# Optimization experiments

Measured on AMD Instinct MI355X. Metric: run time of the kernel, lower is better.

## Reference

```python
import jax, jax.numpy as jnp
import numpy as np

N_EMBD = 1024
N_HEAD = 16
HEAD_DIM = N_EMBD // N_HEAD


def _linear_params(key, fan_in, fan_out):
    kw, kb = jax.random.split(key)
    bound = 1.0 / np.sqrt(fan_in)
    W = jax.random.uniform(kw, (fan_out, fan_in), minval=-bound, maxval=bound, dtype=jnp.float32)
    b = jax.random.uniform(kb, (fan_out,), minval=-bound, maxval=bound, dtype=jnp.float32)
    return W, b


def setup_inputs() -> dict:
    key = jax.random.key(0)
    ks = jax.random.split(key, 7)
    B, T, C = 4, 2048, N_EMBD
    k = jax.random.normal(ks[0], (B, T, C), dtype=jnp.float32)
    q = jax.random.normal(ks[1], (B, T, C), dtype=jnp.float32)
    v = jax.random.normal(ks[2], (B, T, C), dtype=jnp.float32)
    Wk, bk = _linear_params(ks[3], C, C)
    Wq, bq = _linear_params(ks[4], C, C)
    Wv, bv = _linear_params(ks[5], C, C)
    Wo, bo = _linear_params(ks[6], C, C)
    return {"k": k, "q": q, "v": v, "Wk": Wk, "bk": bk, "Wq": Wq, "bq": bq,
            "Wv": Wv, "bv": bv, "Wo": Wo, "bo": bo}


def reference(k, q, v, Wk, bk, Wq, bq, Wv, bv, Wo, bo):
    B, T, C = k.shape
    H, CH = N_HEAD, C // N_HEAD
    # projections (nn.Linear: x @ W.T + b), split heads -> [b, h, t, ch]
    keys = (k @ Wk.T + bk).reshape(B, T, H, CH).transpose(0, 2, 1, 3)
    queries = (q @ Wq.T + bq).reshape(B, T, H, CH).transpose(0, 2, 1, 3)
    values = (v @ Wv.T + bv).reshape(B, T, H, CH).transpose(0, 2, 1, 3)
    # [b, h, t, t] scores, scaled before softmax as in the original
    att = jnp.einsum('bhqd,bhkd->bhqk', queries, keys)
    att = jax.nn.softmax(att * (CH ** -0.5), axis=-1)
    out = jnp.einsum('bhqk,bhkd->bhqd', att, values)
    out = out.transpose(0, 2, 1, 3).reshape(B, T, C)
    return out @ Wo.T + bo
```

## Files before the change

### kernel.cpp

```cpp
#include <hip/hip_runtime.h>


typedef short bf8 __attribute__((ext_vector_type(8)));
typedef float f4 __attribute__((ext_vector_type(4)));
typedef float f16v __attribute__((ext_vector_type(16)));
typedef unsigned short u16;

#define AS1 __attribute__((address_space(1)))
#define AS3 __attribute__((address_space(3)))

__device__ __forceinline__ u16 f2b(float f) {
  unsigned u = __builtin_bit_cast(unsigned, f);
  u += 0x7FFFu + ((u >> 16) & 1u);
  return (u16)(u >> 16);
}

__device__ __forceinline__ unsigned cvtpk(float lo, float hi) {
  unsigned r;
  asm("v_cvt_pk_bf16_f32 %0, %1, %2" : "=v"(r) : "v"(lo), "v"(hi));
  return r;
}

__device__ __forceinline__ void swap32(unsigned& a, unsigned& b) {
  asm("v_permlane32_swap_b32 %0, %1" : "+v"(a), "+v"(b));
}

__global__ void cvt4_kernel(const float* __restrict__ a, const float* __restrict__ b,
                            const float* __restrict__ c, const float* __restrict__ d,
                            u16* __restrict__ out) {
  int i = blockIdx.x * blockDim.x + threadIdx.x;
  const int sel = i >> 18, off = i & 0x3FFFF;
  const float* src = sel == 0 ? a : sel == 1 ? b : sel == 2 ? c : d;
  float4 f = ((const float4*)src)[off];
  ushort4 o;
  o.x = f2b(f.x); o.y = f2b(f.y); o.z = f2b(f.z); o.w = f2b(f.w);
  ((ushort4*)out)[i] = o;
}

template<int MODE>
__device__ __forceinline__ void gemm_epilogue(
    f4 (&acc)[4][4], const float* __restrict__ bias, void* __restrict__ Cout,
    int N, float scale, int m0, int n0, int wm, int wn, int lr, int lg)
{
  if (MODE == 0) {
    float bv[4];
    #pragma unroll
    for (int j = 0; j < 4; ++j) bv[j] = bias[n0 + wn + j * 16 + lr];
    float* C = (float*)Cout;
    #pragma unroll
    for (int i = 0; i < 4; ++i)
      #pragma unroll
      for (int j = 0; j < 4; ++j) {
        const int col = n0 + wn + j * 16 + lr;
        #pragma unroll
        for (int r = 0; r < 4; ++r) {
          const int row = m0 + wm + i * 16 + lg * 4 + r;
          C[(size_t)row * N + col] = acc[i][j][r] + bv[j];
        }
      }
  } else if (MODE == 1) {
    float bv[4];
    #pragma unroll
    for (int j = 0; j < 4; ++j) bv[j] = bias[n0 + wn + j * 16 + lr];
    u16* C = (u16*)Cout;
    #pragma unroll
    for (int i = 0; i < 4; ++i)
      #pragma unroll
      for (int j = 0; j < 4; ++j) {
        const int col = n0 + wn + j * 16 + lr;
        const int h = col >> 6, ch = col & 63;
        #pragma unroll
        for (int r = 0; r < 4; ++r) {
          const int row = m0 + wm + i * 16 + lg * 4 + r;
          const int b = row >> 11, t = row & 2047;
          C[((size_t)(b * 16 + h) * 2048 + t) * 64 + ch] = f2b((acc[i][j][r] + bv[j]) * scale);
        }
      }
  } else {
    u16* C = (u16*)Cout;
    #pragma unroll
    for (int i = 0; i < 4; ++i)
      #pragma unroll
      for (int r = 0; r < 4; ++r) {
        const int nch = m0 + wm + i * 16 + lg * 4 + r;
        const float br = bias[nch];
        const int h = nch >> 6, ch = nch & 63;
        #pragma unroll
        for (int j = 0; j < 4; ++j) {
          const int tok = n0 + wn + j * 16 + lr;
          const int b = tok >> 11, t = tok & 2047;
          C[((size_t)((b * 16 + h) * 64 + ch) << 11) + t] = f2b(acc[i][j][r] + br);
        }
      }
  }
}

template<int MODE, int ACTB>
__device__ __forceinline__ void gemm_fp_body(
    u16* __restrict__ actT, u16* __restrict__ wT,
    const float* __restrict__ act, const u16* __restrict__ Wt,
    const float* __restrict__ bias, void* __restrict__ Cout,
    int N, int K, float scale, int m0, int n0)
{
  const int tid = threadIdx.x, lane = tid & 63, w = tid >> 6;
  const int wm = (w >> 1) << 6, wn = (w & 1) << 6;
  const int lr = lane & 15, lg = lane >> 4;
  const int arow0 = (ACTB ? n0 : m0);
  const int wrow0 = (ACTB ? m0 : n0);

  f4 acc[4][4] = {};
  float4 ta[8];

  #pragma unroll
  for (int q = 0; q < 4; ++q) {
    const int c = (w << 8) + (q << 6) + lane;
    const int row = c >> 3, col = (c & 7) << 3;
    const float* s = act + (size_t)(arow0 + row) * K + col;
    ta[2 * q] = *(const float4*)s; ta[2 * q + 1] = *(const float4*)(s + 4);
  }
  #pragma unroll
  for (int q = 0; q < 4; ++q) {
    const int c = (w << 8) + (q << 6) + lane;
    const int row = c >> 3, sw = ((c & 7) ^ (row & 7)) << 3;
    __builtin_amdgcn_global_load_lds(
        (const AS1 void*)(Wt + (size_t)(wrow0 + row) * K + sw),
        (AS3 void*)(wT + (((w << 2) + q) << 9)), 16, 0, 0);
  }
  #pragma unroll
  for (int q = 0; q < 4; ++q) {
    const int c = (w << 8) + (q << 6) + lane;
    const int row = c >> 3;
    uint4 pk;
    pk.x = cvtpk(ta[2 * q].x, ta[2 * q].y);
    pk.y = cvtpk(ta[2 * q].z, ta[2 * q].w);
    pk.z = cvtpk(ta[2 * q + 1].x, ta[2 * q + 1].y);
    pk.w = cvtpk(ta[2 * q + 1].z, ta[2 * q + 1].w);
    *(uint4*)(actT + (row << 6) + (((c & 7) ^ (row & 7)) << 3)) = pk;
  }
  #pragma unroll
  for (int q = 0; q < 4; ++q) {
    const int c = (w << 8) + (q << 6) + lane;
    const int row = c >> 3, col = (c & 7) << 3;
    const float* s = act + (size_t)(arow0 + row) * K + 64 + col;
    ta[2 * q] = *(const float4*)s; ta[2 * q + 1] = *(const float4*)(s + 4);
  }
  __syncthreads();

  const int NKT = K >> 6;
  for (int kt = 0; kt < NKT; ++kt) {
    const int cur = kt & 1;
    const u16* aC = actT + (cur << 13);
    const u16* wC = wT + (cur << 13);
    if (kt + 1 < NKT) {
      u16* aN = actT + ((cur ^ 1) << 13);
      u16* wN = wT + ((cur ^ 1) << 13);
      const int k1 = (kt + 1) << 6;
      #pragma unroll
      for (int q = 0; q < 4; ++q) {
        const int c = (w << 8) + (q << 6) + lane;
        const int row = c >> 3, sw = ((c & 7) ^ (row & 7)) << 3;
        __builtin_amdgcn_global_load_lds(
            (const AS1 void*)(Wt + (size_t)(wrow0 + row) * K + k1 + sw),
            (AS3 void*)(wN + (((w << 2) + q) << 9)), 16, 0, 0);
      }
      #pragma unroll
      for (int q = 0; q < 4; ++q) {
        const int c = (w << 8) + (q << 6) + lane;
        const int row = c >> 3;
        uint4 pk;
        pk.x = cvtpk(ta[2 * q].x, ta[2 * q].y);
        pk.y = cvtpk(ta[2 * q].z, ta[2 * q].w);
        pk.z = cvtpk(ta[2 * q + 1].x, ta[2 * q + 1].y);
        pk.w = cvtpk(ta[2 * q + 1].z, ta[2 * q + 1].w);
        *(uint4*)(aN + (row << 6) + (((c & 7) ^ (row & 7)) << 3)) = pk;
      }
      if (kt + 2 < NKT) {
        const int k2 = (kt + 2) << 6;
        #pragma unroll
        for (int q = 0; q < 4; ++q) {
          const int c = (w << 8) + (q << 6) + lane;
          const int row = c >> 3, col = (c & 7) << 3;
          const float* s = act + (size_t)(arow0 + row) * K + k2 + col;
          ta[2 * q] = *(const float4*)s; ta[2 * q + 1] = *(const float4*)(s + 4);
        }
      }
    }
    #pragma unroll
    for (int ks = 0; ks < 2; ++ks) {
      bf8 af[4], bfr[4];
      #pragma unroll
      for (int i = 0; i < 4; ++i) {
        const int ra = wm + i * 16 + lr;
        const int rb = wn + i * 16 + lr;
        const u16* aSrc = ACTB ? wC : aC;
        const u16* bSrc = ACTB ? aC : wC;
        af[i]  = *(const bf8*)(aSrc + (ra << 6) + ((((ks << 2) + lg) ^ (ra & 7)) << 3));
        bfr[i] = *(const bf8*)(bSrc + (rb << 6) + ((((ks << 2) + lg) ^ (rb & 7)) << 3));
      }
      __builtin_amdgcn_s_setprio(1);
      #pragma unroll
      for (int i = 0; i < 4; ++i)
        #pragma unroll
        for (int j = 0; j < 4; ++j)
          acc[i][j] = __builtin_amdgcn_mfma_f32_16x16x32_bf16(af[i], bfr[j], acc[i][j], 0, 0, 0);
      __builtin_amdgcn_s_setprio(0);
    }
    __syncthreads();
  }

  gemm_epilogue<MODE>(acc, bias, Cout, N, scale, m0, n0, wm, wn, lr, lg);
}

__global__ __launch_bounds__(256, 2)
void proj_qkv(const float* __restrict__ q_in, const float* __restrict__ k_in,
              const float* __restrict__ v_in,
              const u16* __restrict__ Wq, const u16* __restrict__ Wk,
              const u16* __restrict__ Wv,
              const float* __restrict__ bq, const float* __restrict__ bk,
              const float* __restrict__ bv,
              u16* __restrict__ Qp, u16* __restrict__ Kp, u16* __restrict__ Vt,
              float qscale)
{
  __shared__ __align__(16) u16 pool[32768];
  u16* const actT = pool;
  u16* const wT   = pool + 16384;

  const int cpx = gridDim.x >> 3;
  const int bid = (blockIdx.x & 7) * cpx + (blockIdx.x >> 3);
  const int which = bid >> 9, sub = bid & 511;

  if (which < 2) {
    gemm_fp_body<1, 0>(actT, wT,
                       which ? k_in : q_in,
                       which ? Wk : Wq,
                       which ? bk : bq,
                       which ? (void*)Kp : (void*)Qp,
                       1024, 1024, which ? 1.f : qscale,
                       (sub >> 3) << 7, (sub & 7) << 7);
  } else {
    gemm_fp_body<2, 1>(actT, wT, v_in, Wv, bv, (void*)Vt,
                       8192, 1024, 1.f, (sub & 7) << 7, (sub >> 3) << 7);
  }
}

__global__ __launch_bounds__(256, 2)
void gemm_out(const u16* __restrict__ A, const u16* __restrict__ B,
              const float* __restrict__ bias, float* __restrict__ C)
{
  __shared__ __align__(16) u16 pool[32768];
  u16* const aT = pool;
  u16* const bT = pool + 16384;

  const int cpx = gridDim.x >> 3;
  const int bid = (blockIdx.x & 7) * cpx + (blockIdx.x >> 3);
  const int m0 = (bid >> 3) << 7, n0 = (bid & 7) << 7;
  const int tid = threadIdx.x, lane = tid & 63, w = tid >> 6;
  const int wm = (w >> 1) << 6, wn = (w & 1) << 6;
  const int lr = lane & 15, lg = lane >> 4;
  const int K = 1024;

  f4 acc[4][4] = {};

  #pragma unroll
  for (int q = 0; q < 4; ++q) {
    const int c = (w << 8) + (q << 6) + lane;
    const int row = c >> 3, sw = ((c & 7) ^ (row & 7)) << 3;
    __builtin_amdgcn_global_load_lds(
        (const AS1 void*)(A + (size_t)(m0 + row) * K + sw),
        (AS3 void*)(aT + (((w << 2) + q) << 9)), 16, 0, 0);
    __builtin_amdgcn_global_load_lds(
        (const AS1 void*)(B + (size_t)(n0 + row) * K + sw),
        (AS3 void*)(bT + (((w << 2) + q) << 9)), 16, 0, 0);
  }
  __syncthreads();

  for (int kt = 0; kt < 16; ++kt) {
    const int cur = kt & 1;
    const u16* aC = aT + (cur << 13);
    const u16* bC = bT + (cur << 13);
    if (kt + 1 < 16) {
      u16* aN = aT + ((cur ^ 1) << 13);
      u16* bN = bT + ((cur ^ 1) << 13);
      const int k1 = (kt + 1) << 6;
      #pragma unroll
      for (int q = 0; q < 4; ++q) {
        const int c = (w << 8) + (q << 6) + lane;
        const int row = c >> 3, sw = ((c & 7) ^ (row & 7)) << 3;
        __builtin_amdgcn_global_load_lds(
            (const AS1 void*)(A + (size_t)(m0 + row) * K + k1 + sw),
            (AS3 void*)(aN + (((w << 2) + q) << 9)), 16, 0, 0);
        __builtin_amdgcn_global_load_lds(
            (const AS1 void*)(B + (size_t)(n0 + row) * K + k1 + sw),
            (AS3 void*)(bN + (((w << 2) + q) << 9)), 16, 0, 0);
      }
    }
    #pragma unroll
    for (int ks = 0; ks < 2; ++ks) {
      bf8 af[4], bfr[4];
      #pragma unroll
      for (int i = 0; i < 4; ++i) {
        const int ra = wm + i * 16 + lr;
        const int rb = wn + i * 16 + lr;
        af[i]  = *(const bf8*)(aC + (ra << 6) + ((((ks << 2) + lg) ^ (ra & 7)) << 3));
        bfr[i] = *(const bf8*)(bC + (rb << 6) + ((((ks << 2) + lg) ^ (rb & 7)) << 3));
      }
      __builtin_amdgcn_s_setprio(1);
      #pragma unroll
      for (int i = 0; i < 4; ++i)
        #pragma unroll
        for (int j = 0; j < 4; ++j)
          acc[i][j] = __builtin_amdgcn_mfma_f32_16x16x32_bf16(af[i], bfr[j], acc[i][j], 0, 0, 0);
      __builtin_amdgcn_s_setprio(0);
    }
    __syncthreads();
  }

  gemm_epilogue<0>(acc, bias, (void*)C, 1024, 1.f, m0, n0, wm, wn, lr, lg);
}

__global__ __launch_bounds__(256, 3)
void attn_kernel(const u16* __restrict__ Qp, const u16* __restrict__ Kp,
                 const u16* __restrict__ VT, u16* __restrict__ Ob)
{
  __shared__ __align__(16) u16 pool[24576];
  u16* const ktb = pool;
  u16* const vtb = pool + 12288;

  const int flat = blockIdx.x;
  const int xcd = flat & 7, idx = flat >> 3;
  const int bh = (xcd << 3) + (idx >> 4);
  const int tq0 = (idx & 15) << 7;

  const int tid = threadIdx.x, lane = tid & 63, w = tid >> 6;
  const int ql = lane & 31, hi = lane >> 5;
  const size_t hoff = (size_t)bh * (2048 * 64);
  const u16* Kh = Kp + hoff;
  const u16* Vh = VT + hoff;

  bf8 qf[4];
  {
    const u16* qp_ = Qp + hoff + (size_t)(tq0 + w * 32 + ql) * 64 + hi * 8;
    #pragma unroll
    for (int ks = 0; ks < 4; ++ks) qf[ks] = *(const bf8*)(qp_ + 16 * ks);
  }

  f16v o0 = {}, o1 = {};
  float lrun = 0.f;

  const int c0i = (w << 7) + lane;
  const int c1i = c0i + 64;
  const int sr0 = c0i >> 3, ss0 = ((c0i & 7) ^ (sr0 & 7)) << 3;
  const int sr1 = c1i >> 3, ss1 = ((c1i & 7) ^ (sr1 & 7)) << 3;
  const int sd0 = (w << 10);
  const int sd1 = (w << 10) + 512;

  #define STAGE(buf, t0)                                                          \
    do {                                                                           \
      __builtin_amdgcn_global_load_lds((const AS1 void*)(Kh + (size_t)((t0) + sr0) * 64 + ss0), \
                                       (AS3 void*)(ktb + (buf) * 4096 + sd0), 16, 0, 0);  \
      __builtin_amdgcn_global_load_lds((const AS1 void*)(Kh + (size_t)((t0) + sr1) * 64 + ss1), \
                                       (AS3 void*)(ktb + (buf) * 4096 + sd1), 16, 0, 0);  \
      __builtin_amdgcn_global_load_lds((const AS1 void*)(Vh + (size_t)sr0 * 2048 + (t0) + ss0), \
                                       (AS3 void*)(vtb + (buf) * 4096 + sd0), 16, 0, 0);  \
      __builtin_amdgcn_global_load_lds((const AS1 void*)(Vh + (size_t)sr1 * 2048 + (t0) + ss1), \
                                       (AS3 void*)(vtb + (buf) * 4096 + sd1), 16, 0, 0);  \
    } while (0)

  STAGE(0, 0);
  STAGE(1, 64);

  const int xq = ql & 7;
  int bc = 0;
  for (int it = 0; it < 32; ++it) {
    if (it < 31) asm volatile("s_waitcnt vmcnt(4)" ::: "memory");
    else         asm volatile("s_waitcnt vmcnt(0)" ::: "memory");
    __builtin_amdgcn_s_barrier();
    __builtin_amdgcn_sched_barrier(0);

    if (it + 2 < 32) {
      const int bs = bc ? bc - 1 : 2;
      STAGE(bs, (it + 2) << 6);
    }

    const u16* kb = ktb + bc * 4096;
    const u16* vb = vtb + bc * 4096;

    f16v s0 = {}, s1 = {};
    #pragma unroll
    for (int ks = 0; ks < 4; ++ks) {
      bf8 kf0 = *(const bf8*)(kb + (ql << 6) + ((((ks << 1) + hi) ^ xq) << 3));
      bf8 kf1 = *(const bf8*)(kb + ((32 + ql) << 6) + ((((ks << 1) + hi) ^ xq) << 3));
      __builtin_amdgcn_s_setprio(1);
      s0 = __builtin_amdgcn_mfma_f32_32x32x16_bf16(kf0, qf[ks], s0, 0, 0, 0);
      s1 = __builtin_amdgcn_mfma_f32_32x32x16_bf16(kf1, qf[ks], s1, 0, 0, 0);
      __builtin_amdgcn_s_setprio(0);
    }

    bf8 vf0[4], vf1[4];
    #pragma unroll
    for (int ks = 0; ks < 4; ++ks) {
      vf0[ks] = *(const bf8*)(vb + (ql << 6) + ((((ks << 1) + hi) ^ xq) << 3));
      vf1[ks] = *(const bf8*)(vb + ((32 + ql) << 6) + ((((ks << 1) + hi) ^ xq) << 3));
    }

    float rs = 0.f;

    {
      unsigned wpk[8];
      #pragma unroll
      for (int i = 0; i < 8; ++i) {
        float e0 = __builtin_amdgcn_exp2f(s0[2 * i]);
        float e1 = __builtin_amdgcn_exp2f(s0[2 * i + 1]);
        rs += e0 + e1;
        wpk[i] = cvtpk(e0, e1);
      }
      swap32(wpk[0], wpk[2]); swap32(wpk[1], wpk[3]);
      swap32(wpk[4], wpk[6]); swap32(wpk[5], wpk[7]);
      bf8 pf0 = __builtin_bit_cast(bf8, make_uint4(wpk[0], wpk[1], wpk[2], wpk[3]));
      bf8 pf1 = __builtin_bit_cast(bf8, make_uint4(wpk[4], wpk[5], wpk[6], wpk[7]));
      __builtin_amdgcn_s_setprio(1);
      o0 = __builtin_amdgcn_mfma_f32_32x32x16_bf16(vf0[0], pf0, o0, 0, 0, 0);
      o1 = __builtin_amdgcn_mfma_f32_32x32x16_bf16(vf1[0], pf0, o1, 0, 0, 0);
      o0 = __builtin_amdgcn_mfma_f32_32x32x16_bf16(vf0[1], pf1, o0, 0, 0, 0);
      o1 = __builtin_amdgcn_mfma_f32_32x32x16_bf16(vf1[1], pf1, o1, 0, 0, 0);
      __builtin_amdgcn_s_setprio(0);
    }

    {
      unsigned wpk[8];
      #pragma unroll
      for (int i = 0; i < 8; ++i) {
        float e0 = __builtin_amdgcn_exp2f(s1[2 * i]);
        float e1 = __builtin_amdgcn_exp2f(s1[2 * i + 1]);
        rs += e0 + e1;
        wpk[i] = cvtpk(e0, e1);
      }
      swap32(wpk[0], wpk[2]); swap32(wpk[1], wpk[3]);
      swap32(wpk[4], wpk[6]); swap32(wpk[5], wpk[7]);
      bf8 pf2 = __builtin_bit_cast(bf8, make_uint4(wpk[0], wpk[1], wpk[2], wpk[3]));
      bf8 pf3 = __builtin_bit_cast(bf8, make_uint4(wpk[4], wpk[5], wpk[6], wpk[7]));
      __builtin_amdgcn_s_setprio(1);
      o0 = __builtin_amdgcn_mfma_f32_32x32x16_bf16(vf0[2], pf2, o0, 0, 0, 0);
      o1 = __builtin_amdgcn_mfma_f32_32x32x16_bf16(vf1[2], pf2, o1, 0, 0, 0);
      o0 = __builtin_amdgcn_mfma_f32_32x32x16_bf16(vf0[3], pf3, o0, 0, 0, 0);
      o1 = __builtin_amdgcn_mfma_f32_32x32x16_bf16(vf1[3], pf3, o1, 0, 0, 0);
      __builtin_amdgcn_s_setprio(0);
    }

    lrun += rs;
    bc = bc + 1 < 3 ? bc + 1 : 0;
  }
  #undef STAGE

  const float linv = 1.f / (lrun + __shfl_xor(lrun, 32));

  __syncthreads();
  u16* const ot = pool;
  const int orow = w * 32 + ql;
  #pragma unroll
  for (int c = 0; c < 2; ++c) {
    const f16v& o = c ? o1 : o0;
    #pragma unroll
    for (int g = 0; g < 4; ++g) {
      uint2 pk;
      pk.x = cvtpk(o[4 * g + 0] * linv, o[4 * g + 1] * linv);
      pk.y = cvtpk(o[4 * g + 2] * linv, o[4 * g + 3] * linv);
      *(uint2*)(ot + orow * 72 + 32 * c + 8 * g + 4 * hi) = pk;
    }
  }
  __syncthreads();

  const int b = bh >> 4, h = bh & 15;
  const int row = tid >> 1, seg = tid & 1;
  const u16* src = ot + row * 72 + seg * 32;
  u16* dst = Ob + ((size_t)(b * 2048 + tq0 + row) * 16 + h) * 64 + seg * 32;
  #pragma unroll
  for (int kk = 0; kk < 4; ++kk)
    *(uint4*)(dst + 8 * kk) = *(const uint4*)(src + 8 * kk);
}

extern "C" void kernel_launch(void* const* d_in, const int* in_sizes, int n_in,
                              void* d_out, int out_size, void* d_ws, size_t ws_size,
                              hipStream_t stream) {
  (void)in_sizes; (void)n_in; (void)out_size; (void)ws_size;
  const float* k_in = (const float*)d_in[0];
  const float* q_in = (const float*)d_in[1];
  const float* v_in = (const float*)d_in[2];
  const float* Wk = (const float*)d_in[3]; const float* bk = (const float*)d_in[4];
  const float* Wq = (const float*)d_in[5]; const float* bq = (const float*)d_in[6];
  const float* Wv = (const float*)d_in[7]; const float* bv = (const float*)d_in[8];
  const float* Wo = (const float*)d_in[9]; const float* bo = (const float*)d_in[10];
  float* out = (float*)d_out;

  char* ws = (char*)d_ws;
  const size_t SZ_ACT = (size_t)8192 * 1024 * 2;
  const size_t SZ_W   = (size_t)1024 * 1024 * 2;
  u16* Oc  = (u16*)(ws);
  u16* Qp  = (u16*)(ws + 1 * SZ_ACT);
  u16* Kp  = (u16*)(ws + 2 * SZ_ACT);
  u16* Vt  = (u16*)(ws + 3 * SZ_ACT);
  u16* Wqb = (u16*)(ws + 4 * SZ_ACT);
  u16* Wkb = (u16*)(ws + 4 * SZ_ACT + SZ_W);
  u16* Wvb = (u16*)(ws + 4 * SZ_ACT + 2 * SZ_W);
  u16* Wob = (u16*)(ws + 4 * SZ_ACT + 3 * SZ_W);

  cvt4_kernel<<<4096, 256, 0, stream>>>(Wq, Wk, Wv, Wo, Wqb);

  const float c0 = 0.125f * 1.4426950408889634f;

  proj_qkv<<<1536, 256, 0, stream>>>(q_in, k_in, v_in, Wqb, Wkb, Wvb,
                                     bq, bk, bv, Qp, Kp, Vt, c0);

  attn_kernel<<<1024, 256, 0, stream>>>(Qp, Kp, Vt, Oc);

  gemm_out<<<512, 256, 0, stream>>>(Oc, Wob, bo, out);
}
```

Baseline: 182.6 us.

## Rework GEMM mainloop pipeline with explicit waitcnts and one barrier per tile

Restructures the projection GEMM K-loop. Each iteration now waits with explicit vmcnt/lgkmcnt counts and a raw s_barrier, then issues the next weight global-to-LDS prefetch before the MFMAs. The fp32-to-bf16 activation conversion and LDS store, plus the next activation load, move to after the MFMA block. The aim is to cut the full __syncthreads drain and let the MFMAs overlap with the outstanding loads. The hand-written waitcnt counts are fragile: if the instruction order shifts, the counts can wait too little or too much.

```diff
diff --git a/kernel.cpp b/kernel.cpp
--- a/kernel.cpp
+++ b/kernel.cpp
@@ -111,80 +111,69 @@
   f4 acc[4][4] = {};
   float4 ta[8];
 
-  #pragma unroll
-  for (int q = 0; q < 4; ++q) {
-    const int c = (w << 8) + (q << 6) + lane;
-    const int row = c >> 3, col = (c & 7) << 3;
-    const float* s = act + (size_t)(arow0 + row) * K + col;
-    ta[2 * q] = *(const float4*)s; ta[2 * q + 1] = *(const float4*)(s + 4);
-  }
-  #pragma unroll
-  for (int q = 0; q < 4; ++q) {
-    const int c = (w << 8) + (q << 6) + lane;
-    const int row = c >> 3, sw = ((c & 7) ^ (row & 7)) << 3;
-    __builtin_amdgcn_global_load_lds(
-        (const AS1 void*)(Wt + (size_t)(wrow0 + row) * K + sw),
-        (AS3 void*)(wT + (((w << 2) + q) << 9)), 16, 0, 0);
-  }
-  #pragma unroll
-  for (int q = 0; q < 4; ++q) {
-    const int c = (w << 8) + (q << 6) + lane;
-    const int row = c >> 3;
-    uint4 pk;
-    pk.x = cvtpk(ta[2 * q].x, ta[2 * q].y);
-    pk.y = cvtpk(ta[2 * q].z, ta[2 * q].w);
-    pk.z = cvtpk(ta[2 * q + 1].x, ta[2 * q + 1].y);
-    pk.w = cvtpk(ta[2 * q + 1].z, ta[2 * q + 1].w);
-    *(uint4*)(actT + (row << 6) + (((c & 7) ^ (row & 7)) << 3)) = pk;
-  }
-  #pragma unroll
-  for (int q = 0; q < 4; ++q) {
-    const int c = (w << 8) + (q << 6) + lane;
-    const int row = c >> 3, col = (c & 7) << 3;
-    const float* s = act + (size_t)(arow0 + row) * K + 64 + col;
-    ta[2 * q] = *(const float4*)s; ta[2 * q + 1] = *(const float4*)(s + 4);
-  }
-  __syncthreads();
+  #define W_GLDS(buf, karg)                                                     \
+    do {                                                                        \
+      const int k_ = (karg);                                                    \
+      u16* dst = wT + ((buf) << 13);                                            \
+      _Pragma("unroll")                                                         \
+      for (int q = 0; q < 4; ++q) {                                             \
+        const int c = (w << 8) + (q << 6) + lane;                               \
+        const int row = c >> 3, sw = ((c & 7) ^ (row & 7)) << 3;                \
+        __builtin_amdgcn_global_load_lds(                                       \
+            (const AS1 void*)(Wt + (size_t)(wrow0 + row) * K + k_ + sw),        \
+            (AS3 void*)(dst + (((w << 2) + q) << 9)), 16, 0, 0);                \
+      }                                                                         \
+    } while (0)
+
+  #define ACT_LOAD(karg)                                                        \
+    do {                                                                        \
+      const int k_ = (karg);                                                    \
+      _Pragma("unroll")                                                         \
+      for (int q = 0; q < 4; ++q) {                                             \
+        const int c = (w << 8) + (q << 6) + lane;                               \
+        const int row = c >> 3, col = (c & 7) << 3;                             \
+        const float* s = act + (size_t)(arow0 + row) * K + k_ + col;            \
+        ta[2 * q] = *(const float4*)s;                                          \
+        ta[2 * q + 1] = *(const float4*)(s + 4);                                \
+      }                                                                         \
+    } while (0)
+
+  #define ACT_WRITE(buf)                                                        \
+    do {                                                                        \
+      u16* dst = actT + ((buf) << 13);                                          \
+      _Pragma("unroll")                                                         \
+      for (int q = 0; q < 4; ++q) {                                             \
+        const int c = (w << 8) + (q << 6) + lane;                               \
+        const int row = c >> 3;                                                 \
+        uint4 pk;                                                               \
+        pk.x = cvtpk(ta[2 * q].x, ta[2 * q].y);                                 \
+        pk.y = cvtpk(ta[2 * q].z, ta[2 * q].w);                                 \
+        pk.z = cvtpk(ta[2 * q + 1].x, ta[2 * q + 1].y);                         \
+        pk.w = cvtpk(ta[2 * q + 1].z, ta[2 * q + 1].w);                         \
+        *(uint4*)(dst + (row << 6) + (((c & 7) ^ (row & 7)) << 3)) = pk;        \
+      }                                                                         \
+    } while (0)
+
+  W_GLDS(0, 0);
+  ACT_LOAD(0);
+  ACT_WRITE(0);
+  ACT_LOAD(64);
+  asm volatile("s_waitcnt lgkmcnt(0)" ::: "memory");
 
   const int NKT = K >> 6;
   for (int kt = 0; kt < NKT; ++kt) {
     const int cur = kt & 1;
+    if (kt > 0) {
+      if (kt + 1 < NKT) asm volatile("s_waitcnt vmcnt(8)" ::: "memory");
+      else              asm volatile("s_waitcnt vmcnt(0)" ::: "memory");
+    }
+    __builtin_amdgcn_s_barrier();
+    __builtin_amdgcn_sched_barrier(0);
+
+    if (kt + 1 < NKT) W_GLDS(cur ^ 1, (kt + 1) << 6);
+
     const u16* aC = actT + (cur << 13);
     const u16* wC = wT + (cur << 13);
-    if (kt + 1 < NKT) {
-      u16* aN = actT + ((cur ^ 1) << 13);
-      u16* wN = wT + ((cur ^ 1) << 13);
-      const int k1 = (kt + 1) << 6;
-      #pragma unroll
-      for (int q = 0; q < 4; ++q) {
-        const int c = (w << 8) + (q << 6) + lane;
-        const int row = c >> 3, sw = ((c & 7) ^ (row & 7)) << 3;
-        __builtin_amdgcn_global_load_lds(
-            (const AS1 void*)(Wt + (size_t)(wrow0 + row) * K + k1 + sw),
-            (AS3 void*)(wN + (((w << 2) + q) << 9)), 16, 0, 0);
-      }
-      #pragma unroll
-      for (int q = 0; q < 4; ++q) {
-        const int c = (w << 8) + (q << 6) + lane;
-        const int row = c >> 3;
-        uint4 pk;
-        pk.x = cvtpk(ta[2 * q].x, ta[2 * q].y);
-        pk.y = cvtpk(ta[2 * q].z, ta[2 * q].w);
-        pk.z = cvtpk(ta[2 * q + 1].x, ta[2 * q + 1].y);
-        pk.w = cvtpk(ta[2 * q + 1].z, ta[2 * q + 1].w);
-        *(uint4*)(aN + (row << 6) + (((c & 7) ^ (row & 7)) << 3)) = pk;
-      }
-      if (kt + 2 < NKT) {
-        const int k2 = (kt + 2) << 6;
-        #pragma unroll
-        for (int q = 0; q < 4; ++q) {
-          const int c = (w << 8) + (q << 6) + lane;
-          const int row = c >> 3, col = (c & 7) << 3;
-          const float* s = act + (size_t)(arow0 + row) * K + k2 + col;
-          ta[2 * q] = *(const float4*)s; ta[2 * q + 1] = *(const float4*)(s + 4);
-        }
-      }
-    }
     #pragma unroll
     for (int ks = 0; ks < 2; ++ks) {
       bf8 af[4], bfr[4];
@@ -205,8 +194,16 @@
           acc[i][j] = __builtin_amdgcn_mfma_f32_16x16x32_bf16(af[i], bfr[j], acc[i][j], 0, 0, 0);
       __builtin_amdgcn_s_setprio(0);
     }
-    __syncthreads();
-  }
+
+    if (kt + 1 < NKT) {
+      ACT_WRITE(cur ^ 1);
+      if (kt + 2 < NKT) ACT_LOAD((kt + 2) << 6);
+    }
+    asm volatile("s_waitcnt lgkmcnt(0)" ::: "memory");
+  }
+  #undef W_GLDS
+  #undef ACT_LOAD
+  #undef ACT_WRITE
 
   gemm_epilogue<MODE>(acc, bias, Cout, N, scale, m0, n0, wm, wn, lr, lg);
 }
```

New measurement: 179.1 us. Within noise of the previous version (-1.9%).
